# Performance work log

Hardware: AMD Instinct MI355X
Metric: run time of the kernel (lower is better)

Reference implementation:

```python
import jax, jax.numpy as jnp
import numpy as np

D = 256; H = 8; HD = D // H; DEPTH = 4
NGRIDS = 512; TILE = 256; IN_CHANS = 1536
MAX_SEQ = (131072 // TILE) ** 2  # 262144
_SEGS = [int(v) for v in 2.0 ** np.linspace(np.log2(1024.0), np.log2(float(MAX_SEQ)), 5)]  # [1024,4096,16384,65536,262144]
_RATIOS = [1, 2, 4, 8, 16]
LN_EPS = 1e-5


def build_pos_embed(dim, gs):
    # MAE-style 2d sincos pos embed with a leading zero row for the cls token.
    def emb1d(d, pos):
        omega = 1.0 / 10000 ** (np.arange(d // 2, dtype=np.float64) / (d / 2.0))
        out = np.einsum('m,d->md', pos.reshape(-1).astype(np.float64), omega)
        return np.concatenate([np.sin(out), np.cos(out)], axis=1)
    g = np.arange(gs, dtype=np.float64)
    gw, gh = np.meshgrid(g, g)  # meshgrid(grid_w, grid_h) as in MAE
    emb = np.concatenate([emb1d(dim // 2, gw), emb1d(dim // 2, gh)], axis=1)  # (gs*gs, dim)
    return np.concatenate([np.zeros((1, dim)), emb], axis=0).astype(np.float32)


def _ln(x, w, b):
    mu = x.mean(-1, keepdims=True)
    var = ((x - mu) ** 2).mean(-1, keepdims=True)
    return (x - mu) * jax.lax.rsqrt(var + LN_EPS) * w + b


def _dilated_attn(x, wqkv, bqkv, wo, bo):
    # LongNet dilated attention: for each (segment_len w, dilation r) branch,
    # attend within segments over a per-head strided subsample (offset = head % r),
    # then combine branches weighted by softmax log-sum-exp.
    B, L, _ = x.shape
    q, k, v = jnp.split(x @ wqkv + bqkv, 3, axis=-1)
    q = q.reshape(B, L, H, HD); k = k.reshape(B, L, H, HD); v = v.reshape(B, L, H, HD)
    scale = 1.0 / np.sqrt(HD)
    outs, lses = [], []
    for w_seg, r in zip(_SEGS, _RATIOS):
        we = min(w_seg, L); we = max((we // r) * r, r)   # effective segment length
        Lp = -(-L // we) * we; pad = Lp - L; n = Lp // we; m = we // r
        idx = (jnp.arange(H) % r)[:, None] + r * jnp.arange(m)[None, :]  # (H, m) per-head strided idx
        def seg(t):
            tp = jnp.pad(t, ((0, 0), (0, pad), (0, 0), (0, 0)))
            tp = tp.reshape(B, n, we, H, HD).transpose(0, 1, 3, 2, 4)  # (B,n,H,we,HD)
            return jnp.take_along_axis(tp, idx[None, None, :, :, None], axis=3)  # (B,n,H,m,HD)
        qs, ks, vs = seg(q), seg(k), seg(v)
        valid = (jnp.arange(Lp) < L).reshape(n, we)[:, idx]  # (n,H,m) key validity (padding mask)
        s = jnp.einsum('bnhqd,bnhkd->bnhqk', qs, ks) * scale
        s = jnp.where(valid[None, :, :, None, :], s, -jnp.inf)
        mx = jnp.maximum(jnp.max(s, axis=-1, keepdims=True), -1e30)
        p = jnp.exp(s - mx)
        den = jnp.sum(p, axis=-1, keepdims=True)
        o = jnp.einsum('bnhqk,bnhkd->bnhqd', p, vs) / jnp.maximum(den, 1e-30)
        lse = mx[..., 0] + jnp.log(jnp.maximum(den[..., 0], 1e-30))  # (B,n,H,m)
        hidx = jnp.arange(H)[:, None]
        of = jnp.zeros((B, n, H, we, HD), x.dtype).at[:, :, hidx, idx].set(o)
        lf = jnp.full((B, n, H, we), -jnp.inf, x.dtype).at[:, :, hidx, idx].set(lse)
        outs.append(of.transpose(0, 1, 3, 2, 4).reshape(B, Lp, H, HD)[:, :L])
        lses.append(lf.transpose(0, 1, 3, 2).reshape(B, Lp, H)[:, :L])
    lse_all = jnp.stack(lses)                         # (S,B,L,H)
    out_all = jnp.stack(outs)                         # (S,B,L,H,HD)
    wgt = jnp.exp(lse_all - jnp.max(lse_all, axis=0, keepdims=True))
    o = jnp.sum(wgt[..., None] * out_all, axis=0) / jnp.sum(wgt, axis=0)[..., None]
    return o.reshape(B, L, D) @ wo + bo


def _forward(x, coords, patch_w, patch_b, cls_token, pos_embed, ln1_w, ln1_b, wqkv, bqkv,
             wo, bo, ln2_w, ln2_b, w1, b1, w2, b2, encln_w, encln_b, norm_w, norm_b):
    B = x.shape[0]
    h = x @ patch_w + patch_b                                   # patch embed (Linear)
    g = jnp.floor(coords / TILE)
    pos = (g[..., 0] * NGRIDS + g[..., 1]).astype(jnp.int32) + 1  # coords_to_pos
    h = h + pos_embed[pos]                                      # irregular pos-embed gather
    cls = jnp.broadcast_to(cls_token + pos_embed[0], (B, 1, D))
    h = jnp.concatenate([cls, h], axis=1)                       # (B, 4096, D)

    def step(hc, p):
        l1w, l1b, qw, qb, ow, ob, l2w, l2b, f1w, f1b, f2w, f2b = p
        hc = hc + _dilated_attn(_ln(hc, l1w, l1b), qw, qb, ow, ob)
        f = jax.nn.gelu(_ln(hc, l2w, l2b) @ f1w + f1b, approximate=False) @ f2w + f2b
        return hc + f, None

    h, _ = jax.lax.scan(step, h, (ln1_w, ln1_b, wqkv, bqkv, wo, bo, ln2_w, ln2_b, w1, b1, w2, b2))
    h = _ln(h, encln_w, encln_b)          # encoder final LN (pre-LN stack)
    return _ln(h, norm_w, norm_b)[:, 0]   # global_pool=False: normed cls token, (B, D)


def setup_inputs() -> dict:
    key = jax.random.key(0)
    ks = jax.random.split(key, 8)
    B, N = 1, 4095
    s = 0.02
    rn = lambda k, shape: jax.random.normal(k, shape, jnp.float32) * s
    return dict(
        x=jax.random.normal(ks[0], (B, N, IN_CHANS), jnp.float32),
        coords=jax.random.randint(ks[1], (B, N, 2), 0, TILE * NGRIDS).astype(jnp.float32),
        patch_w=rn(ks[2], (IN_CHANS, D)), patch_b=jnp.zeros((D,), jnp.float32),
        cls_token=rn(ks[3], (1, 1, D)),
        pos_embed=jnp.asarray(build_pos_embed(D, NGRIDS)),
        ln1_w=jnp.ones((DEPTH, D), jnp.float32), ln1_b=jnp.zeros((DEPTH, D), jnp.float32),
        wqkv=rn(ks[4], (DEPTH, D, 3 * D)), bqkv=jnp.zeros((DEPTH, 3 * D), jnp.float32),
        wo=rn(ks[5], (DEPTH, D, D)), bo=jnp.zeros((DEPTH, D), jnp.float32),
        ln2_w=jnp.ones((DEPTH, D), jnp.float32), ln2_b=jnp.zeros((DEPTH, D), jnp.float32),
        w1=rn(ks[6], (DEPTH, D, 4 * D)), b1=jnp.zeros((DEPTH, 4 * D), jnp.float32),
        w2=rn(ks[7], (DEPTH, 4 * D, D)), b2=jnp.zeros((DEPTH, D), jnp.float32),
        encln_w=jnp.ones((D,), jnp.float32), encln_b=jnp.zeros((D,), jnp.float32),
        norm_w=jnp.ones((D,), jnp.float32), norm_b=jnp.zeros((D,), jnp.float32),
    )


def reference(x, coords, patch_w, patch_b, cls_token, pos_embed, ln1_w, ln1_b, wqkv, bqkv,
              wo, bo, ln2_w, ln2_b, w1, b1, w2, b2, encln_w, encln_b, norm_w, norm_b):
    return _forward(x, coords, patch_w, patch_b, cls_token, pos_embed, ln1_w, ln1_b, wqkv, bqkv,
                    wo, bo, ln2_w, ln2_b, w1, b1, w2, b2, encln_w, encln_b, norm_w, norm_b)
```

## Files before the change

### kernel.cpp

```cpp
#include <hip/hip_runtime.h>
#include <hip/hip_bf16.h>
#include <math.h>


typedef __attribute__((ext_vector_type(8))) short short8;
typedef __attribute__((ext_vector_type(4))) float f32x4;

__device__ __forceinline__ float wred_sum(float v) {
#pragma unroll
  for (int o = 32; o; o >>= 1) v += __shfl_xor(v, o);
  return v;
}

__device__ __forceinline__ unsigned short f2bf(float x) {
  unsigned u = __float_as_uint(x);
  u += 0x7FFF + ((u >> 16) & 1);
  return (unsigned short)(u >> 16);
}
__device__ __forceinline__ float bf2f(unsigned short s) {
  return __uint_as_float(((unsigned)s) << 16);
}

__global__ __launch_bounds__(256) void prep_kernel(
    const float* __restrict__ pw, const float* __restrict__ wqkv,
    const float* __restrict__ wo, const float* __restrict__ w1,
    const float* __restrict__ w2, unsigned short* __restrict__ wt,
    const float* __restrict__ x, unsigned short* __restrict__ xb) {
  __shared__ float T[32][33];
  if (blockIdx.x >= 3456) {
    const int i = (blockIdx.x - 3456) * 256 + threadIdx.x;
    const int row = i / 192, k8 = i % 192;
    const int k = k8 * 8;
    size_t dst = ((size_t)(row >> 4) * 48 + (k >> 5)) * 512 +
                 (size_t)(row & 15) * 32 + (k & 31);
    if (row >= 4095) {
      *(uint4*)(xb + dst) = make_uint4(0, 0, 0, 0);
      return;
    }
    const float4 a = *(const float4*)(x + (size_t)row * 1536 + k);
    const float4 b = *(const float4*)(x + (size_t)row * 1536 + k + 4);
    unsigned u0 = (unsigned)f2bf(a.x) | ((unsigned)f2bf(a.y) << 16);
    unsigned u1 = (unsigned)f2bf(a.z) | ((unsigned)f2bf(a.w) << 16);
    unsigned u2 = (unsigned)f2bf(b.x) | ((unsigned)f2bf(b.y) << 16);
    unsigned u3 = (unsigned)f2bf(b.z) | ((unsigned)f2bf(b.w) << 16);
    *(uint4*)(xb + dst) = make_uint4(u0, u1, u2, u3);
    return;
  }
  const int bid = blockIdx.x;
  const float* src;
  int Kd, Nd, lt;
  size_t doff;
  if (bid < 384) {
    src = pw; Kd = 1536; Nd = 256; doff = 0; lt = bid;
  } else if (bid < 1152) {
    int l = (bid - 384) / 192, r = (bid - 384) % 192;
    src = wqkv + (size_t)l * 196608; Kd = 256; Nd = 768;
    doff = 393216 + (size_t)l * 196608; lt = r;
  } else if (bid < 1408) {
    int l = (bid - 1152) / 64, r = (bid - 1152) % 64;
    src = wo + (size_t)l * 65536; Kd = 256; Nd = 256;
    doff = 1179648 + (size_t)l * 65536; lt = r;
  } else if (bid < 2432) {
    int l = (bid - 1408) / 256, r = (bid - 1408) % 256;
    src = w1 + (size_t)l * 262144; Kd = 256; Nd = 1024;
    doff = 1441792 + (size_t)l * 262144; lt = r;
  } else {
    int l = (bid - 2432) / 256, r = (bid - 2432) % 256;
    src = w2 + (size_t)l * 262144; Kd = 1024; Nd = 256;
    doff = 2490368 + (size_t)l * 262144; lt = r;
  }
  const int tilesK = Kd >> 5;
  const int tn = lt / tilesK, tk = lt % tilesK;
  const int k0 = tk * 32, n0 = tn * 32;
  const int t = threadIdx.x;
  const int rr = t >> 3, c4 = t & 7;
  float4 v = *(const float4*)(src + (size_t)(k0 + rr) * Nd + n0 + c4 * 4);
  T[rr][c4 * 4 + 0] = v.x;
  T[rr][c4 * 4 + 1] = v.y;
  T[rr][c4 * 4 + 2] = v.z;
  T[rr][c4 * 4 + 3] = v.w;
  __syncthreads();
  float o0 = T[c4 * 4 + 0][rr], o1 = T[c4 * 4 + 1][rr];
  float o2 = T[c4 * 4 + 2][rr], o3 = T[c4 * 4 + 3][rr];
  unsigned u0 = (unsigned)f2bf(o0) | ((unsigned)f2bf(o1) << 16);
  unsigned u1 = (unsigned)f2bf(o2) | ((unsigned)f2bf(o3) << 16);
  const int n = n0 + rr;
  size_t fo = doff + ((size_t)(n >> 4) * (Kd >> 5) + (k0 >> 5)) * 512 +
              (size_t)(n & 15) * 32 + c4 * 4;
  *(uint2*)(wt + fo) = make_uint2(u0, u1);
}

__global__ __launch_bounds__(256) void gemm_patch(
    const unsigned short* __restrict__ Af, const unsigned short* __restrict__ Bt,
    const float* __restrict__ bias, const float* __restrict__ coords,
    const float* __restrict__ cls, const float* __restrict__ pe,
    float* __restrict__ h) {
  const int lane = threadIdx.x & 63, w = threadIdx.x >> 6;
  const int g = lane >> 4, q = lane & 15;
  const int bm = blockIdx.x * 64, bn = blockIdx.y * 32;

  const unsigned short* ap =
      Af + ((size_t)((bm >> 4) + w) * 48) * 512 + q * 32 + 8 * g;
  const unsigned short* bp = Bt + q * 32 + 8 * g;

  f32x4 acc[2];
#pragma unroll
  for (int i = 0; i < 2; i++) acc[i] = (f32x4){0.f, 0.f, 0.f, 0.f};

#pragma unroll 4
  for (int ks = 0; ks < 48; ks++) {
    short8 af = *(const short8*)(ap + (size_t)ks * 512);
#pragma unroll
    for (int cf = 0; cf < 2; cf++) {
      short8 bf = *(const short8*)(bp +
          ((size_t)(((bn >> 4) + cf) * 48 + ks)) * 512);
      acc[cf] = __builtin_amdgcn_mfma_f32_16x16x32_bf16(af, bf, acc[cf], 0, 0, 0);
    }
  }

  const int orow0 = bm + 16 * w + 4 * g;
  int prow[4];
#pragma unroll
  for (int rg = 0; rg < 4; rg++) {
    int orow = orow0 + rg;
    orow = orow < 4095 ? orow : 4094;
    float c0 = coords[(size_t)orow * 2 + 0];
    float c1 = coords[(size_t)orow * 2 + 1];
    prow[rg] = (int)floorf(c0 * (1.f / 256.f)) * 512 +
               (int)floorf(c1 * (1.f / 256.f)) + 1;
  }
#pragma unroll
  for (int cf = 0; cf < 2; cf++) {
    const int col = bn + 16 * cf + q;
    const float bs = bias[col];
#pragma unroll
    for (int rg = 0; rg < 4; rg++) {
      int orow = orow0 + rg;
      if (orow < 4095) {
        float c = acc[cf][rg] + bs + pe[(size_t)prow[rg] * 256 + col];
        h[(size_t)(orow + 1) * 256 + col] = c;
      }
    }
  }
  if (blockIdx.x == 0 && blockIdx.y == 0 && threadIdx.x < 64) {
    float4 cv = *(const float4*)(cls + threadIdx.x * 4);
    float4 pv = *(const float4*)(pe + threadIdx.x * 4);
    *(float4*)(h + threadIdx.x * 4) =
        make_float4(cv.x + pv.x, cv.y + pv.y, cv.z + pv.z, cv.w + pv.w);
  }
}

__global__ __launch_bounds__(256) void ln_bf16_kernel(
    const float* __restrict__ x, const float* __restrict__ wg,
    const float* __restrict__ b, unsigned short* __restrict__ y) {
  const int row = blockIdx.x * 4 + (threadIdx.x >> 6);
  const int lane = threadIdx.x & 63;
  float4 v = *(const float4*)(x + (size_t)row * 256 + lane * 4);
  float s1 = wred_sum(v.x + v.y + v.z + v.w);
  float s2 = wred_sum(v.x * v.x + v.y * v.y + v.z * v.z + v.w * v.w);
  float mu = s1 * (1.f / 256.f);
  float inv = rsqrtf(s2 * (1.f / 256.f) - mu * mu + 1e-5f);
  float4 wv = *(const float4*)(wg + lane * 4);
  float4 bv = *(const float4*)(b + lane * 4);
  float o0 = (v.x - mu) * inv * wv.x + bv.x;
  float o1 = (v.y - mu) * inv * wv.y + bv.y;
  float o2 = (v.z - mu) * inv * wv.z + bv.z;
  float o3 = (v.w - mu) * inv * wv.w + bv.w;
  unsigned u0 = (unsigned)f2bf(o0) | ((unsigned)f2bf(o1) << 16);
  unsigned u1 = (unsigned)f2bf(o2) | ((unsigned)f2bf(o3) << 16);
  size_t addr = ((size_t)(row >> 4) * 8 + (lane >> 3)) * 512 +
                (size_t)(row & 15) * 32 + (lane & 7) * 4;
  *(uint2*)(y + addr) = make_uint2(u0, u1);
}

template <int EPI>
__global__ __launch_bounds__(512) void gemm_af(
    const unsigned short* __restrict__ Af, const unsigned short* __restrict__ Bt,
    const float* __restrict__ bias, unsigned short* __restrict__ Cv, int N) {
  const int lane = threadIdx.x & 63, w = threadIdx.x >> 6;
  const int g = lane >> 4, q = lane & 15;
  const int bm = blockIdx.x * 128, bn = blockIdx.y * 32;
  const unsigned short* ap =
      Af + ((size_t)((bm >> 4) + w) * 8) * 512 + q * 32 + 8 * g;
  const unsigned short* bp = Bt + q * 32 + 8 * g;

  f32x4 acc[2];
#pragma unroll
  for (int i = 0; i < 2; i++) acc[i] = (f32x4){0.f, 0.f, 0.f, 0.f};

#pragma unroll
  for (int ks = 0; ks < 8; ks++) {
    short8 af = *(const short8*)(ap + (size_t)ks * 512);
#pragma unroll
    for (int cf = 0; cf < 2; cf++) {
      short8 bf = *(const short8*)(bp +
          ((size_t)((bn >> 4) + cf) * 8 + ks) * 512);
      acc[cf] = __builtin_amdgcn_mfma_f32_16x16x32_bf16(af, bf, acc[cf], 0, 0, 0);
    }
  }

  const int orow0 = bm + 16 * w + 4 * g;
#pragma unroll
  for (int cf = 0; cf < 2; cf++) {
    const int col = bn + 16 * cf + q;
    const float bs = bias[col];
#pragma unroll
    for (int rg = 0; rg < 4; rg++) {
      float c = acc[cf][rg] + bs;
      const int orow = orow0 + rg;
      if (EPI == 1) {
        c = 0.5f * c * (1.f + erff(c * 0.70710678118654752f));
        const int cq = 16 * cf + q;
        size_t idx = ((size_t)(orow >> 4) * (N >> 5) + (bn >> 5) + (cq >> 5)) *
                         512 +
                     (size_t)(orow & 15) * 32 + (cq & 31);
        Cv[idx] = f2bf(c);
      } else {
        Cv[(size_t)orow * N + col] = f2bf(c);
      }
    }
  }
}

__global__ __launch_bounds__(256) void gemm_proj(
    const unsigned short* __restrict__ Af, const unsigned short* __restrict__ Bt,
    const float* __restrict__ bias, float* __restrict__ C) {
  const int lane = threadIdx.x & 63, w = threadIdx.x >> 6;
  const int g = lane >> 4, q = lane & 15;
  const int bm = blockIdx.x * 64, bn = blockIdx.y * 32;
  const unsigned short* ap =
      Af + ((size_t)((bm >> 4) + w) * 8) * 512 + q * 32 + 8 * g;
  const unsigned short* bp = Bt + q * 32 + 8 * g;

  f32x4 acc[2];
#pragma unroll
  for (int i = 0; i < 2; i++) acc[i] = (f32x4){0.f, 0.f, 0.f, 0.f};

#pragma unroll
  for (int ks = 0; ks < 8; ks++) {
    short8 af = *(const short8*)(ap + (size_t)ks * 512);
#pragma unroll
    for (int cf = 0; cf < 2; cf++) {
      short8 bf = *(const short8*)(bp +
          ((size_t)((bn >> 4) + cf) * 8 + ks) * 512);
      acc[cf] = __builtin_amdgcn_mfma_f32_16x16x32_bf16(af, bf, acc[cf], 0, 0, 0);
    }
  }

  const int orow0 = bm + 16 * w + 4 * g;
#pragma unroll
  for (int cf = 0; cf < 2; cf++) {
    const int col = bn + 16 * cf + q;
    const float bs = bias[col];
#pragma unroll
    for (int rg = 0; rg < 4; rg++)
      C[(size_t)(orow0 + rg) * 256 + col] += acc[cf][rg] + bs;
  }
}

__global__ __launch_bounds__(256) void gemm_mlp2(
    const unsigned short* __restrict__ Af, const unsigned short* __restrict__ Bt,
    const float* __restrict__ bias, float* __restrict__ C) {
  const int lane = threadIdx.x & 63, w = threadIdx.x >> 6;
  const int g = lane >> 4, q = lane & 15;
  const int bm = blockIdx.x * 64, bn = blockIdx.y * 32;
  const unsigned short* ap =
      Af + ((size_t)((bm >> 4) + w) * 32) * 512 + q * 32 + 8 * g;
  const unsigned short* bp = Bt + q * 32 + 8 * g;

  f32x4 acc[2];
#pragma unroll
  for (int i = 0; i < 2; i++) acc[i] = (f32x4){0.f, 0.f, 0.f, 0.f};

#pragma unroll 4
  for (int ks = 0; ks < 32; ks++) {
    short8 af = *(const short8*)(ap + (size_t)ks * 512);
#pragma unroll
    for (int cf = 0; cf < 2; cf++) {
      short8 bf = *(const short8*)(bp +
          ((size_t)((bn >> 4) + cf) * 32 + ks) * 512);
      acc[cf] = __builtin_amdgcn_mfma_f32_16x16x32_bf16(af, bf, acc[cf], 0, 0, 0);
    }
  }

  const int orow0 = bm + 16 * w + 4 * g;
#pragma unroll
  for (int cf = 0; cf < 2; cf++) {
    const int col = bn + 16 * cf + q;
    const float bs = bias[col];
#pragma unroll
    for (int rg = 0; rg < 4; rg++)
      C[(size_t)(orow0 + rg) * 256 + col] += acc[cf][rg] + bs;
  }
}

__device__ __forceinline__ void decode_gather(int bid, int& r, int& m,
                                              int& off, int& base, int& h,
                                              int& kt, int& ub) {
  const int c = bid & 7;
  const int j = bid >> 3;
  if (j < 64) {
    int u = c + 8 * (j >> 4);
    kt = j & 15;
    r = 1; m = 1024; base = (u >> 3) * 1024; h = u & 7; off = 0; ub = u * 32768;
  } else if (j < 96) {
    int jj = j - 64;
    int grp = c + 8 * (jj >> 4);
    h = grp >> 1;
    kt = (grp & 1) * 16 + (jj & 15);
    r = 2; m = 2048; base = 0; off = h & 1; ub = 1048576 + h * 65536;
  } else if (j < 112) {
    h = c; kt = j - 96;
    r = 4; m = 1024; base = 0; off = h & 3; ub = 1572864 + h * 32768;
  } else if (j < 120) {
    h = c; kt = j - 112;
    r = 8; m = 512; base = 0; off = h & 7; ub = 1835008 + h * 16384;
  } else {
    h = c; kt = j - 120;
    r = 16; m = 256; base = 0; off = h; ub = 1966080 + h * 8192;
  }
}

__global__ __launch_bounds__(256) void gather_kernel(
    const unsigned short* __restrict__ qkvb, unsigned short* __restrict__ kg,
    unsigned short* __restrict__ vt) {
  __shared__ unsigned short T[32][64];
  int r, m, off, base, h, kt, ub;
  decode_gather(blockIdx.x, r, m, off, base, h, kt, ub);
  const int t = threadIdx.x;
  {
    int key = t >> 2, c = t & 3;
    size_t row = base + off + (size_t)r * (kt * 64 + key);
    const unsigned short* src = qkvb + row * 768 + h * 32 + 8 * c;
    short8 kk = *(const short8*)(src + 256);
    int gk = kt * 64 + key;
    *(short8*)(kg + ub + (size_t)(gk >> 4) * 512 + (size_t)(gk & 15) * 32 +
               8 * c) = kk;
    short8 vv = *(const short8*)(src + 512);
#pragma unroll
    for (int i = 0; i < 8; i++) T[8 * c + i][key] = (unsigned short)vv[i];
  }
  __syncthreads();
  int dim = t >> 3, c8 = t & 7;
  int vk = kt * 64 + 8 * c8;
  *(short8*)(vt + ub + ((size_t)(vk >> 5) * 2 + (dim >> 4)) * 512 +
             (size_t)(dim & 15) * 32 + (vk & 31)) = *(const short8*)&T[dim][8 * c8];
}

__device__ __forceinline__ void decode_attn(int bid, int& slot, int& r, int& m,
                                            int& nt, int& koff, int& off,
                                            int& base, int& h, int& qt,
                                            int& ub) {
  const int c = bid & 7;
  const int j = bid >> 3;
  if (j < 64) {
    int u = c + 8 * (j >> 4);
    qt = j & 15;
    slot = 0; r = 1; m = 1024; nt = 16; koff = 0;
    base = (u >> 3) * 1024; h = u & 7; off = 0; ub = u * 32768;
  } else if (j < 128) {
    int jj = j - 64;
    int grp = c + 8 * (jj >> 5);
    h = grp >> 1;
    int half = grp & 1;
    qt = jj & 31;
    slot = 1 + half; r = 2; m = 2048; nt = 16; koff = half * 1024;
    base = 0; off = h & 1; ub = 1048576 + h * 65536;
  } else if (j < 144) {
    h = c; qt = j - 128;
    slot = 3; r = 4; m = 1024; nt = 16; koff = 0;
    base = 0; off = h & 3; ub = 1572864 + h * 32768;
  } else if (j < 152) {
    h = c; qt = j - 144;
    slot = 4; r = 8; m = 512; nt = 8; koff = 0;
    base = 0; off = h & 7; ub = 1835008 + h * 16384;
  } else {
    h = c; qt = j - 152;
    slot = 5; r = 16; m = 256; nt = 4; koff = 0;
    base = 0; off = h; ub = 1966080 + h * 8192;
  }
}

__global__ __launch_bounds__(256) void attn_mfma_kernel(
    const unsigned short* __restrict__ qkvb,
    const unsigned short* __restrict__ kg, const unsigned short* __restrict__ vt,
    unsigned short* __restrict__ oa, float* __restrict__ rl_all) {
  int slot, r, m, nt, koff, off, base, h, qt, ub;
  decode_attn(blockIdx.x, slot, r, m, nt, koff, off, base, h, qt, ub);

  const int lane = threadIdx.x & 63;
  const int wid = threadIdx.x >> 6;
  const int g = lane >> 4, q = lane & 15;
  const int q0 = qt * 64 + wid * 16;

  const size_t qrow = base + off + (size_t)r * (q0 + q);
  short8 qf = *(const short8*)(qkvb + qrow * 768 + h * 32 + 8 * g);

  const unsigned short* kp = kg + ub + q * 32 + 8 * g;
  const unsigned short* vp = vt + ub + q * 32 + 8 * g;
  const int kt0 = koff >> 4;
  const int vt0 = koff >> 5;

  f32x4 ot0 = {0.f, 0.f, 0.f, 0.f}, ot1 = {0.f, 0.f, 0.f, 0.f};
  float rl = 0.f;
  const float scale = 0.17677669529663687f;

  short8 kf[4];
#pragma unroll
  for (int a = 0; a < 4; a++)
    kf[a] = *(const short8*)(kp + (size_t)(kt0 + a) * 512);

  for (int kt = 0; kt < nt; ++kt) {
    const int k0 = kt * 64;
    const int v2 = vt0 + (k0 >> 5);
    short8 va0 = *(const short8*)(vp + (size_t)(v2 * 2 + 0) * 512);
    short8 vb0 = *(const short8*)(vp + (size_t)(v2 * 2 + 1) * 512);
    short8 va1 = *(const short8*)(vp + (size_t)((v2 + 1) * 2 + 0) * 512);
    short8 vb1 = *(const short8*)(vp + (size_t)((v2 + 1) * 2 + 1) * 512);

    f32x4 st[4];
#pragma unroll
    for (int a = 0; a < 4; a++) {
      f32x4 z = {0.f, 0.f, 0.f, 0.f};
      st[a] = __builtin_amdgcn_mfma_f32_16x16x32_bf16(kf[a], qf, z, 0, 0, 0);
    }
    if (kt + 1 < nt) {
#pragma unroll
      for (int a = 0; a < 4; a++)
        kf[a] = *(const short8*)(kp + (size_t)(kt0 + ((k0 + 64) >> 4) + a) * 512);
    }

    float p[4][4];
    float tl = 0.f;
#pragma unroll
    for (int a = 0; a < 4; a++)
#pragma unroll
      for (int rr = 0; rr < 4; rr++) {
        p[a][rr] = __expf(st[a][rr] * scale);
        tl += p[a][rr];
      }
    tl += __shfl_xor(tl, 16);
    tl += __shfl_xor(tl, 32);
    rl += tl;

    unsigned pk[4][2];
#pragma unroll
    for (int a = 0; a < 4; a++) {
      asm("v_cvt_pk_bf16_f32 %0, %1, %2"
          : "=v"(pk[a][0]) : "v"(p[a][0]), "v"(p[a][1]));
      asm("v_cvt_pk_bf16_f32 %0, %1, %2"
          : "=v"(pk[a][1]) : "v"(p[a][2]), "v"(p[a][3]));
    }

#pragma unroll
    for (int kk = 0; kk < 2; kk++) {
      union { unsigned w[4]; short8 v; } pb;
#pragma unroll
      for (int jj = 0; jj < 2; jj++) {
        int src = q + 16 * ((2 * g + jj) & 3);
#pragma unroll
        for (int d = 0; d < 2; d++) {
          unsigned lo = (unsigned)__shfl((int)pk[2 * kk + 0][d], src);
          unsigned hi = (unsigned)__shfl((int)pk[2 * kk + 1][d], src);
          pb.w[jj * 2 + d] = (g >> 1) ? hi : lo;
        }
      }
      if (kk == 0) {
        ot0 = __builtin_amdgcn_mfma_f32_16x16x32_bf16(va0, pb.v, ot0, 0, 0, 0);
        ot1 = __builtin_amdgcn_mfma_f32_16x16x32_bf16(vb0, pb.v, ot1, 0, 0, 0);
      } else {
        ot0 = __builtin_amdgcn_mfma_f32_16x16x32_bf16(va1, pb.v, ot0, 0, 0, 0);
        ot1 = __builtin_amdgcn_mfma_f32_16x16x32_bf16(vb1, pb.v, ot1, 0, 0, 0);
      }
    }
  }

  int pos = base + off + r * (q0 + q);
  size_t ob = (((size_t)(slot * 256 + (pos >> 4)) * 8 + h) * 16 + (pos & 15)) * 32;
  unsigned w0 = (unsigned)f2bf(ot0[0]) | ((unsigned)f2bf(ot0[1]) << 16);
  unsigned w1 = (unsigned)f2bf(ot0[2]) | ((unsigned)f2bf(ot0[3]) << 16);
  unsigned w2 = (unsigned)f2bf(ot1[0]) | ((unsigned)f2bf(ot1[1]) << 16);
  unsigned w3 = (unsigned)f2bf(ot1[2]) | ((unsigned)f2bf(ot1[3]) << 16);
  *(uint2*)(oa + ob + 4 * g) = make_uint2(w0, w1);
  *(uint2*)(oa + ob + 16 + 4 * g) = make_uint2(w2, w3);
  if (g == 0)
    rl_all[((size_t)slot * 4096 + pos) * 8 + h] = rl;
}

__global__ __launch_bounds__(256) void combine_kernel(
    const unsigned short* __restrict__ oa, const float* __restrict__ rl_all,
    unsigned short* __restrict__ attb) {
  __shared__ float ls[6][16];
  const int pt = blockIdx.x >> 3, ph = blockIdx.x & 7;
  const int t = threadIdx.x;
  const int d0 = (t & 15) * 2;
  const int pl = t >> 4;
  const int pos = pt * 16 + pl;

  const int msk[6] = {0, 1, 1, 3, 7, 15};
  if (t < 96) {
    int s = t >> 4, p = t & 15;
    int ps = pt * 16 + p;
    bool cov = ((ps ^ ph) & msk[s]) == 0;
    ls[s][p] = cov ? rl_all[((size_t)s * 4096 + ps) * 8 + ph] : 0.f;
  }
  __syncthreads();

  float wsum = 0.f, o0 = 0.f, o1 = 0.f;
#pragma unroll
  for (int s = 0; s < 6; s++) {
    if (((pos ^ ph) & msk[s]) == 0) {
      wsum += ls[s][pl];
      unsigned u = *(const unsigned*)(oa +
          (((size_t)(s * 256 + pt) * 8 + ph) * 16 + pl) * 32 + d0);
      o0 += bf2f((unsigned short)(u & 0xFFFF));
      o1 += bf2f((unsigned short)(u >> 16));
    }
  }
  float inv = 1.f / wsum;
  unsigned u = (unsigned)f2bf(o0 * inv) | ((unsigned)f2bf(o1 * inv) << 16);
  *(unsigned*)(attb + ((size_t)pt * 8 + ph) * 512 + pl * 32 + d0) = u;
}

__global__ __launch_bounds__(64) void final_kernel(
    const float* __restrict__ h, const float* __restrict__ ew,
    const float* __restrict__ eb, const float* __restrict__ nw,
    const float* __restrict__ nb, float* __restrict__ out) {
  const int lane = threadIdx.x;
  float4 v = *(const float4*)(h + lane * 4);
  float s1 = wred_sum(v.x + v.y + v.z + v.w);
  float s2 = wred_sum(v.x * v.x + v.y * v.y + v.z * v.z + v.w * v.w);
  float mu = s1 * (1.f / 256.f);
  float inv = rsqrtf(s2 * (1.f / 256.f) - mu * mu + 1e-5f);
  float4 wv = *(const float4*)(ew + lane * 4);
  float4 bv = *(const float4*)(eb + lane * 4);
  float4 tv;
  tv.x = (v.x - mu) * inv * wv.x + bv.x;
  tv.y = (v.y - mu) * inv * wv.y + bv.y;
  tv.z = (v.z - mu) * inv * wv.z + bv.z;
  tv.w = (v.w - mu) * inv * wv.w + bv.w;
  s1 = wred_sum(tv.x + tv.y + tv.z + tv.w);
  s2 = wred_sum(tv.x * tv.x + tv.y * tv.y + tv.z * tv.z + tv.w * tv.w);
  mu = s1 * (1.f / 256.f);
  inv = rsqrtf(s2 * (1.f / 256.f) - mu * mu + 1e-5f);
  float4 w2v = *(const float4*)(nw + lane * 4);
  float4 b2v = *(const float4*)(nb + lane * 4);
  float4 o;
  o.x = (tv.x - mu) * inv * w2v.x + b2v.x;
  o.y = (tv.y - mu) * inv * w2v.y + b2v.y;
  o.z = (tv.z - mu) * inv * w2v.z + b2v.z;
  o.w = (tv.w - mu) * inv * w2v.w + b2v.w;
  *(float4*)(out + lane * 4) = o;
}


extern "C" void kernel_launch(void* const* d_in, const int* in_sizes, int n_in,
                              void* d_out, int out_size, void* d_ws,
                              size_t ws_size, hipStream_t stream) {
  const float* x      = (const float*)d_in[0];
  const float* coords = (const float*)d_in[1];
  const float* pw     = (const float*)d_in[2];
  const float* pb     = (const float*)d_in[3];
  const float* cls    = (const float*)d_in[4];
  const float* pe     = (const float*)d_in[5];
  const float* ln1w   = (const float*)d_in[6];
  const float* ln1b   = (const float*)d_in[7];
  const float* wqkv   = (const float*)d_in[8];
  const float* bqkv   = (const float*)d_in[9];
  const float* wo     = (const float*)d_in[10];
  const float* bo     = (const float*)d_in[11];
  const float* ln2w   = (const float*)d_in[12];
  const float* ln2b   = (const float*)d_in[13];
  const float* w1     = (const float*)d_in[14];
  const float* b1     = (const float*)d_in[15];
  const float* w2     = (const float*)d_in[16];
  const float* b2     = (const float*)d_in[17];
  const float* encw   = (const float*)d_in[18];
  const float* encb   = (const float*)d_in[19];
  const float* nw     = (const float*)d_in[20];
  const float* nb     = (const float*)d_in[21];

  float* ws = (float*)d_ws;
  float* h              = ws;
  unsigned short* hnbf  = (unsigned short*)(ws + 1048576);
  unsigned short* qkvb  = (unsigned short*)(ws + 1572864);
  unsigned short* kg    = (unsigned short*)(ws + 3145728);
  unsigned short* vt    = (unsigned short*)(ws + 4161536);
  unsigned short* oa    = (unsigned short*)(ws + 5177344);
  float* rla            = ws + 8323072;
  unsigned short* attb  = (unsigned short*)(ws + 8519680);
  unsigned short* midb  = (unsigned short*)(ws + 9043968);
  unsigned short* xb    = (unsigned short*)(ws + 11141120);
  unsigned short* wt    = (unsigned short*)(ws + 14286848);

  prep_kernel<<<6528, 256, 0, stream>>>(pw, wqkv, wo, w1, w2, wt, x, xb);
  gemm_patch<<<dim3(64, 8), 256, 0, stream>>>(xb, wt, pb, coords, cls, pe, h);

  for (int l = 0; l < 4; l++) {
    ln_bf16_kernel<<<1024, 256, 0, stream>>>(h, ln1w + l * 256, ln1b + l * 256,
                                             hnbf);
    gemm_af<3><<<dim3(32, 24), 512, 0, stream>>>(
        hnbf, wt + 393216 + (size_t)l * 196608, bqkv + l * 768, qkvb, 768);
    gather_kernel<<<992, 256, 0, stream>>>(qkvb, kg, vt);
    attn_mfma_kernel<<<1248, 256, 0, stream>>>(qkvb, kg, vt, oa, rla);
    combine_kernel<<<2048, 256, 0, stream>>>(oa, rla, attb);
    gemm_proj<<<dim3(64, 8), 256, 0, stream>>>(
        attb, wt + 1179648 + (size_t)l * 65536, bo + l * 256, h);
    ln_bf16_kernel<<<1024, 256, 0, stream>>>(h, ln2w + l * 256, ln2b + l * 256,
                                             hnbf);
    gemm_af<1><<<dim3(32, 32), 512, 0, stream>>>(
        hnbf, wt + 1441792 + (size_t)l * 262144, b1 + l * 1024, midb, 1024);
    gemm_mlp2<<<dim3(64, 8), 256, 0, stream>>>(
        midb, wt + 2490368 + (size_t)l * 262144, b2 + l * 256, h);
  }

  final_kernel<<<1, 64, 0, stream>>>(h, encw, encb, nw, nb, (float*)d_out);
}
```

Before: 434.5 us.

## Software-pipeline attention loop so QK MFMA of next tile overlaps softmax

Unrolls the attention key loop by two and double-buffers the K fragments and score tiles, issuing the QK^T MFMAs for the next tile before the exp/PV work of the current one. The aim is to overlap matrix-core latency with the VALU softmax and shuffles instead of running them back to back. This costs more registers (two K fragment sets and two score tiles), which may lower occupancy. It also assumes nt is even, which holds for every decoded branch (16, 8, 4).

```diff
diff --git a/kernel.cpp b/kernel.cpp
--- a/kernel.cpp
+++ b/kernel.cpp
@@ -381,6 +381,56 @@
   }
 }
 
+__device__ __forceinline__ void softmax_tile(const f32x4* st, float p[4][4],
+                                             float& rl) {
+  const float scale = 0.17677669529663687f;
+  float tl = 0.f;
+#pragma unroll
+  for (int a = 0; a < 4; a++)
+#pragma unroll
+    for (int rr = 0; rr < 4; rr++) {
+      p[a][rr] = __expf(st[a][rr] * scale);
+      tl += p[a][rr];
+    }
+  tl += __shfl_xor(tl, 16);
+  tl += __shfl_xor(tl, 32);
+  rl += tl;
+}
+
+__device__ __forceinline__ void pv_tile(const float p[4][4], int q, int g,
+                                        short8 va0, short8 vb0, short8 va1,
+                                        short8 vb1, f32x4& ot0, f32x4& ot1) {
+  unsigned pk[4][2];
+#pragma unroll
+  for (int a = 0; a < 4; a++) {
+    asm("v_cvt_pk_bf16_f32 %0, %1, %2"
+        : "=v"(pk[a][0]) : "v"(p[a][0]), "v"(p[a][1]));
+    asm("v_cvt_pk_bf16_f32 %0, %1, %2"
+        : "=v"(pk[a][1]) : "v"(p[a][2]), "v"(p[a][3]));
+  }
+#pragma unroll
+  for (int kk = 0; kk < 2; kk++) {
+    union { unsigned w[4]; short8 v; } pb;
+#pragma unroll
+    for (int jj = 0; jj < 2; jj++) {
+      int src = q + 16 * ((2 * g + jj) & 3);
+#pragma unroll
+      for (int d = 0; d < 2; d++) {
+        unsigned lo = (unsigned)__shfl((int)pk[2 * kk + 0][d], src);
+        unsigned hi = (unsigned)__shfl((int)pk[2 * kk + 1][d], src);
+        pb.w[jj * 2 + d] = (g >> 1) ? hi : lo;
+      }
+    }
+    if (kk == 0) {
+      ot0 = __builtin_amdgcn_mfma_f32_16x16x32_bf16(va0, pb.v, ot0, 0, 0, 0);
+      ot1 = __builtin_amdgcn_mfma_f32_16x16x32_bf16(vb0, pb.v, ot1, 0, 0, 0);
+    } else {
+      ot0 = __builtin_amdgcn_mfma_f32_16x16x32_bf16(va1, pb.v, ot0, 0, 0, 0);
+      ot1 = __builtin_amdgcn_mfma_f32_16x16x32_bf16(vb1, pb.v, ot1, 0, 0, 0);
+    }
+  }
+}
+
 __global__ __launch_bounds__(256) void attn_mfma_kernel(
     const unsigned short* __restrict__ qkvb,
     const unsigned short* __restrict__ kg, const unsigned short* __restrict__ vt,
@@ -403,75 +453,61 @@
 
   f32x4 ot0 = {0.f, 0.f, 0.f, 0.f}, ot1 = {0.f, 0.f, 0.f, 0.f};
   float rl = 0.f;
-  const float scale = 0.17677669529663687f;
-
-  short8 kf[4];
+  const f32x4 z4 = {0.f, 0.f, 0.f, 0.f};
+
+  short8 kfa[4], kfb[4];
 #pragma unroll
   for (int a = 0; a < 4; a++)
-    kf[a] = *(const short8*)(kp + (size_t)(kt0 + a) * 512);
-
-  for (int kt = 0; kt < nt; ++kt) {
-    const int k0 = kt * 64;
-    const int v2 = vt0 + (k0 >> 5);
-    short8 va0 = *(const short8*)(vp + (size_t)(v2 * 2 + 0) * 512);
-    short8 vb0 = *(const short8*)(vp + (size_t)(v2 * 2 + 1) * 512);
-    short8 va1 = *(const short8*)(vp + (size_t)((v2 + 1) * 2 + 0) * 512);
-    short8 vb1 = *(const short8*)(vp + (size_t)((v2 + 1) * 2 + 1) * 512);
-
-    f32x4 st[4];
-#pragma unroll
-    for (int a = 0; a < 4; a++) {
-      f32x4 z = {0.f, 0.f, 0.f, 0.f};
-      st[a] = __builtin_amdgcn_mfma_f32_16x16x32_bf16(kf[a], qf, z, 0, 0, 0);
-    }
-    if (kt + 1 < nt) {
+    kfa[a] = *(const short8*)(kp + (size_t)(kt0 + a) * 512);
+#pragma unroll
+  for (int a = 0; a < 4; a++)
+    kfb[a] = *(const short8*)(kp + (size_t)(kt0 + 4 + a) * 512);
+
+  f32x4 st[4], stn[4];
+#pragma unroll
+  for (int a = 0; a < 4; a++)
+    st[a] = __builtin_amdgcn_mfma_f32_16x16x32_bf16(kfa[a], qf, z4, 0, 0, 0);
+
+  for (int kt = 0; kt < nt; kt += 2) {
+    {
+      const int k0 = kt * 64;
+      const int v2 = vt0 + (k0 >> 5);
+      short8 va0 = *(const short8*)(vp + (size_t)(v2 * 2 + 0) * 512);
+      short8 vb0 = *(const short8*)(vp + (size_t)(v2 * 2 + 1) * 512);
+      short8 va1 = *(const short8*)(vp + (size_t)((v2 + 1) * 2 + 0) * 512);
+      short8 vb1 = *(const short8*)(vp + (size_t)((v2 + 1) * 2 + 1) * 512);
+      if (kt + 2 < nt) {
+#pragma unroll
+        for (int a = 0; a < 4; a++)
+          kfa[a] = *(const short8*)(kp + (size_t)(kt0 + (kt + 2) * 4 + a) * 512);
+      }
+      float p[4][4];
+      softmax_tile(st, p, rl);
 #pragma unroll
       for (int a = 0; a < 4; a++)
-        kf[a] = *(const short8*)(kp + (size_t)(kt0 + ((k0 + 64) >> 4) + a) * 512);
-    }
-
-    float p[4][4];
-    float tl = 0.f;
-#pragma unroll
-    for (int a = 0; a < 4; a++)
-#pragma unroll
-      for (int rr = 0; rr < 4; rr++) {
-        p[a][rr] = __expf(st[a][rr] * scale);
-        tl += p[a][rr];
+        stn[a] = __builtin_amdgcn_mfma_f32_16x16x32_bf16(kfb[a], qf, z4, 0, 0, 0);
+      pv_tile(p, q, g, va0, vb0, va1, vb1, ot0, ot1);
+    }
+    {
+      const int k0 = (kt + 1) * 64;
+      const int v2 = vt0 + (k0 >> 5);
+      short8 va0 = *(const short8*)(vp + (size_t)(v2 * 2 + 0) * 512);
+      short8 vb0 = *(const short8*)(vp + (size_t)(v2 * 2 + 1) * 512);
+      short8 va1 = *(const short8*)(vp + (size_t)((v2 + 1) * 2 + 0) * 512);
+      short8 vb1 = *(const short8*)(vp + (size_t)((v2 + 1) * 2 + 1) * 512);
+      if (kt + 3 < nt) {
+#pragma unroll
+        for (int a = 0; a < 4; a++)
+          kfb[a] = *(const short8*)(kp + (size_t)(kt0 + (kt + 3) * 4 + a) * 512);
       }
-    tl += __shfl_xor(tl, 16);
-    tl += __shfl_xor(tl, 32);
-    rl += tl;
-
-    unsigned pk[4][2];
-#pragma unroll
-    for (int a = 0; a < 4; a++) {
-      asm("v_cvt_pk_bf16_f32 %0, %1, %2"
-          : "=v"(pk[a][0]) : "v"(p[a][0]), "v"(p[a][1]));
-      asm("v_cvt_pk_bf16_f32 %0, %1, %2"
-          : "=v"(pk[a][1]) : "v"(p[a][2]), "v"(p[a][3]));
-    }
-
-#pragma unroll
-    for (int kk = 0; kk < 2; kk++) {
-      union { unsigned w[4]; short8 v; } pb;
-#pragma unroll
-      for (int jj = 0; jj < 2; jj++) {
-        int src = q + 16 * ((2 * g + jj) & 3);
-#pragma unroll
-        for (int d = 0; d < 2; d++) {
-          unsigned lo = (unsigned)__shfl((int)pk[2 * kk + 0][d], src);
-          unsigned hi = (unsigned)__shfl((int)pk[2 * kk + 1][d], src);
-          pb.w[jj * 2 + d] = (g >> 1) ? hi : lo;
-        }
+      float p[4][4];
+      softmax_tile(stn, p, rl);
+      if (kt + 2 < nt) {
+#pragma unroll
+        for (int a = 0; a < 4; a++)
+          st[a] = __builtin_amdgcn_mfma_f32_16x16x32_bf16(kfa[a], qf, z4, 0, 0, 0);
       }
-      if (kk == 0) {
-        ot0 = __builtin_amdgcn_mfma_f32_16x16x32_bf16(va0, pb.v, ot0, 0, 0, 0);
-        ot1 = __builtin_amdgcn_mfma_f32_16x16x32_bf16(vb0, pb.v, ot1, 0, 0, 0);
-      } else {
-        ot0 = __builtin_amdgcn_mfma_f32_16x16x32_bf16(va1, pb.v, ot0, 0, 0, 0);
-        ot1 = __builtin_amdgcn_mfma_f32_16x16x32_bf16(vb1, pb.v, ot1, 0, 0, 0);
-      }
+      pv_tile(p, q, g, va0, vb0, va1, vb1, ot0, ot1);
     }
   }
 
```

Result: no change. 435.1 us (+0.1%).
